# Kernel optimization log

Hardware: AMD Instinct MI355X
Metric: run time of the kernel (lower is better)

Reference implementation:

```python
import jax, jax.numpy as jnp
import numpy as np

H = 50  # hidden_layer_size

def _lstm_layer(x, Wih, Whh, bih, bhh):
    # x: [B, T, D_in]; Wih: [4H, D_in]; Whh: [4H, H]; biases: [4H]
    # Precompute input contribution to all gates for every timestep.
    xg = jnp.einsum('btd,gd->btg', x, Wih) + bih + bhh  # [B, T, 4H]
    xg = jnp.transpose(xg, (1, 0, 2))                   # [T, B, 4H] for scan
    B = x.shape[0]
    h0 = jnp.zeros((B, H), x.dtype)
    c0 = jnp.zeros((B, H), x.dtype)

    def step(carry, xt):
        h, c = carry
        g = xt + h @ Whh.T                              # [B, 4H]
        i, f, gg, o = jnp.split(g, 4, axis=-1)          # PyTorch gate order i,f,g,o
        i = jax.nn.sigmoid(i)
        f = jax.nn.sigmoid(f)
        gg = jnp.tanh(gg)
        o = jax.nn.sigmoid(o)
        c = f * c + i * gg
        h = o * jnp.tanh(c)
        return (h, c), h

    (_, _), hs = jax.lax.scan(step, (h0, c0), xg)       # hs: [T, B, H]
    return jnp.transpose(hs, (1, 0, 2))                 # [B, T, H]


def setup_inputs() -> dict:
    key = jax.random.key(0)
    ks = jax.random.split(key, 11)
    B, T, D = 4096, 512, 1
    s = 1.0 / np.sqrt(H)  # PyTorch LSTM init scale
    inp = {
        'x': jax.random.normal(ks[0], (B, T, D), jnp.float32),
        'W_ih0': jax.random.uniform(ks[1], (4 * H, D), jnp.float32, -s, s),
        'W_hh0': jax.random.uniform(ks[2], (4 * H, H), jnp.float32, -s, s),
        'b_ih0': jax.random.uniform(ks[3], (4 * H,), jnp.float32, -s, s),
        'b_hh0': jax.random.uniform(ks[4], (4 * H,), jnp.float32, -s, s),
        'W_ih1': jax.random.uniform(ks[5], (4 * H, H), jnp.float32, -s, s),
        'W_hh1': jax.random.uniform(ks[6], (4 * H, H), jnp.float32, -s, s),
        'b_ih1': jax.random.uniform(ks[7], (4 * H,), jnp.float32, -s, s),
        'b_hh1': jax.random.uniform(ks[8], (4 * H,), jnp.float32, -s, s),
        'fc_W': jax.random.uniform(ks[9], (1, H), jnp.float32, -s, s),
        'fc_b': jax.random.uniform(ks[10], (1,), jnp.float32, -s, s),
    }
    return inp


def reference(x, W_ih0, W_hh0, b_ih0, b_hh0, W_ih1, W_hh1, b_ih1, b_hh1, fc_W, fc_b):
    h1 = _lstm_layer(x, W_ih0, W_hh0, b_ih0, b_hh0)     # [B, T, H]
    h2 = _lstm_layer(h1, W_ih1, W_hh1, b_ih1, b_hh1)    # [B, T, H]
    last = h2[:, -1, :]                                 # [B, H]
    return last @ fc_W.T + fc_b                         # [B, 1]
```

## Files before the change

kernel.cpp:

```cpp
#include <hip/hip_runtime.h>


typedef __attribute__((ext_vector_type(8))) _Float16 half8;
typedef __attribute__((ext_vector_type(4))) float f32x4;

#define LOG2E 1.44269504088896340736f

__device__ __forceinline__ float rcp_(float x) { return __builtin_amdgcn_rcpf(x); }
__device__ __forceinline__ float exp2_(float x) { return __builtin_amdgcn_exp2f(x); }
__device__ __forceinline__ float sigm(float x) {
  return rcp_(1.f + exp2_(-LOG2E * x));
}
__device__ __forceinline__ float tanh_(float x) {
  return 1.f - 2.f * rcp_(1.f + exp2_(2.f * LOG2E * x));
}
__device__ __forceinline__ f32x4 mfma16(half8 a, half8 b, f32x4 c) {
  return __builtin_amdgcn_mfma_f32_16x16x32_f16(a, b, c, 0, 0, 0);
}

union ABu16 { uint4 u; half8 v; };
__device__ __forceinline__ half8 rdfrag(const _Float16* p) {
  ABu16 t;
  t.u = *(const uint4*)p;
  return t.v;
}

__device__ __forceinline__ half8 loadW1(const float* __restrict__ W, int n,
                                        int gate, int kbase, int lg) {
  half8 r;
#pragma unroll
  for (int e = 0; e < 8; ++e) {
    const int k = kbase + 16 * (e >> 2) + 4 * lg + (e & 3);
    const bool v = (n < 50) && (k < 50);
    r[e] = (_Float16)(v ? W[(gate * 50 + n) * 50 + k] : 0.f);
  }
  return r;
}

#define GATES(X) X(0) X(1) X(2) X(3)

#define FINR(r, PH, WPc)                                      \
  {                                                           \
    const float i_ = sigm(ai[r]), ff = sigm(af[r]);           \
    const float g_ = tanh_(ag[r]), o_ = sigm(ao[r]);          \
    cc##r = ff * cc##r + i_ * g_;                             \
    PH[WPc][woff + 8 * (r)] = (_Float16)(o_ * tanh_(cc##r));  \
  }

__global__ __launch_bounds__(512) void lstm2_kernel(
    const float* __restrict__ x,
    const float* __restrict__ Wih0, const float* __restrict__ Whh0,
    const float* __restrict__ bih0, const float* __restrict__ bhh0,
    const float* __restrict__ Wih1, const float* __restrict__ Whh1,
    const float* __restrict__ bih1, const float* __restrict__ bhh1,
    const float* __restrict__ fcW, const float* __restrict__ fcb,
    float* __restrict__ out) {
  const int tid = threadIdx.x;
  const int lane = tid & 63;
  const int wv = tid >> 6;
  const int wg = wv & 3;
  const bool isL1 = wv >= 4;
  const int lg = lane >> 4;
  const int l15 = lane & 15;
  const int bbase = blockIdx.x * 16;

  __shared__ __align__(16) _Float16 H0[2][1024], H1[2][1024];
  __shared__ float xs2[64][16];
  __shared__ float ldspad[18688];

  ((volatile float*)ldspad)[tid] = 0.f;

  for (int i = tid; i < 1024; i += 512) {
    ((unsigned int*)H0)[i] = 0u;
    ((unsigned int*)H1)[i] = 0u;
  }

  const int lane8 = lane * 8;
  const int u = 16 * wg + l15;
  const bool uv = (u < 50);
  const int woff = ((u >> 5) << 9) + (((u >> 2) & 3) << 7) + ((4 * lg) << 3) +
                   (((u >> 4) & 1) << 2) + (u & 3);

#define STAGE(c)                                                        \
  {                                                                     \
    const int b_ = tid >> 4, fg_ = tid & 15;                            \
    const float4 v_ = *(const float4*)&x[(size_t)(bbase + b_) * 512 +   \
                                         (c) * 64 + 4 * fg_];           \
    xs2[4 * fg_ + 0][b_] = v_.x; xs2[4 * fg_ + 1][b_] = v_.y;           \
    xs2[4 * fg_ + 2][b_] = v_.z; xs2[4 * fg_ + 3][b_] = v_.w;           \
  }

  if (!isL1) {
#define DECL0(G) half8 W0_##G, W1_##G; float bi_##G = 0.f, wx_##G = 0.f;
    GATES(DECL0)
#define LOAD0(G)                                              \
    { W0_##G = loadW1(Whh0, u, G, 0, lg);                     \
      W1_##G = loadW1(Whh0, u, G, 32, lg);                    \
      if (uv) {                                               \
        bi_##G = bih0[G * 50 + u] + bhh0[G * 50 + u];         \
        wx_##G = Wih0[G * 50 + u];                            \
      } }
    GATES(LOAD0)
    float cc0 = 0.f, cc1 = 0.f, cc2 = 0.f, cc3 = 0.f;

#define MM0(G, ACC)                                           \
    ACC = mfma16(f0, W0_##G, ACC);                            \
    ACC = mfma16(f1, W1_##G, ACC);

#define L0STEP(RP, WP, tm)                                                  \
    { const half8 f0 = rdfrag(&H0[RP][lane8]);                              \
      const half8 f1 = rdfrag(&H0[RP][512 + lane8]);                        \
      const float4 xv = *(const float4*)&xs2[tm][4 * lg];                   \
      f32x4 ai = {fmaf(xv.x, wx_0, bi_0), fmaf(xv.y, wx_0, bi_0),           \
                  fmaf(xv.z, wx_0, bi_0), fmaf(xv.w, wx_0, bi_0)};          \
      f32x4 af = {fmaf(xv.x, wx_1, bi_1), fmaf(xv.y, wx_1, bi_1),           \
                  fmaf(xv.z, wx_1, bi_1), fmaf(xv.w, wx_1, bi_1)};          \
      f32x4 ag = {fmaf(xv.x, wx_2, bi_2), fmaf(xv.y, wx_2, bi_2),           \
                  fmaf(xv.z, wx_2, bi_2), fmaf(xv.w, wx_2, bi_2)};          \
      f32x4 ao = {fmaf(xv.x, wx_3, bi_3), fmaf(xv.y, wx_3, bi_3),           \
                  fmaf(xv.z, wx_3, bi_3), fmaf(xv.w, wx_3, bi_3)};          \
      MM0(0, ai) MM0(1, af) MM0(2, ag) MM0(3, ao)                           \
      FINR(0, H0, WP) FINR(1, H0, WP) FINR(2, H0, WP) FINR(3, H0, WP) }

    STAGE(0) __syncthreads();
    L0STEP(1, 0, 0) __syncthreads();
    for (int it = 0; it < 255; ++it) {
      const int todd = 2 * it + 1;
      L0STEP(0, 1, (todd & 63)) __syncthreads();
      const int tev = todd + 1;
      if ((tev & 63) == 0) { STAGE(tev >> 6) __syncthreads(); }
      L0STEP(1, 0, (tev & 63)) __syncthreads();
    }
    L0STEP(0, 1, 63) __syncthreads();
    __syncthreads();
  } else {
#define DECL1(G) half8 I0_##G, I1_##G, R0_##G, R1_##G; float bi_##G = 0.f;
    GATES(DECL1)
#define LOAD1(G)                                              \
    { I0_##G = loadW1(Wih1, u, G, 0, lg);                     \
      I1_##G = loadW1(Wih1, u, G, 32, lg);                    \
      R0_##G = loadW1(Whh1, u, G, 0, lg);                     \
      R1_##G = loadW1(Whh1, u, G, 32, lg);                    \
      if (uv) bi_##G = bih1[G * 50 + u] + bhh1[G * 50 + u]; }
    GATES(LOAD1)
    float cc0 = 0.f, cc1 = 0.f, cc2 = 0.f, cc3 = 0.f;

#define MM1(G, ACC)                                           \
    ACC = mfma16(f0, I0_##G, ACC);                            \
    ACC = mfma16(f1, I1_##G, ACC);                            \
    ACC = mfma16(g0, R0_##G, ACC);                            \
    ACC = mfma16(g1, R1_##G, ACC);

#define L1STEP(P0, R1p, W1p)                                                \
    { const half8 f0 = rdfrag(&H0[P0][lane8]);                              \
      const half8 f1 = rdfrag(&H0[P0][512 + lane8]);                        \
      const half8 g0 = rdfrag(&H1[R1p][lane8]);                             \
      const half8 g1 = rdfrag(&H1[R1p][512 + lane8]);                       \
      f32x4 ai = {bi_0, bi_0, bi_0, bi_0};                                  \
      f32x4 af = {bi_1, bi_1, bi_1, bi_1};                                  \
      f32x4 ag = {bi_2, bi_2, bi_2, bi_2};                                  \
      f32x4 ao = {bi_3, bi_3, bi_3, bi_3};                                  \
      MM1(0, ai) MM1(1, af) MM1(2, ag) MM1(3, ao)                           \
      FINR(0, H1, W1p) FINR(1, H1, W1p) FINR(2, H1, W1p) FINR(3, H1, W1p) }

    __syncthreads(); __syncthreads();
    for (int it = 0; it < 255; ++it) {
      L1STEP(0, 1, 0) __syncthreads();
      if (((2 * it + 2) & 63) == 0) __syncthreads();
      L1STEP(1, 0, 1) __syncthreads();
    }
    L1STEP(0, 1, 0) __syncthreads();
    L1STEP(1, 0, 1) __syncthreads();
  }

  if (tid < 16) {
    float s = fcb[0];
    for (int j = 0; j < 50; ++j) {
      const int idx = ((j >> 5) << 9) + (((j >> 2) & 3) << 7) + (tid << 3) +
                      (((j >> 4) & 1) << 2) + (j & 3);
      s += fcW[j] * (float)H1[1][idx];
    }
    out[bbase + tid] = s;
  }
}

extern "C" void kernel_launch(void* const* d_in, const int* in_sizes, int n_in,
                              void* d_out, int out_size, void* d_ws, size_t ws_size,
                              hipStream_t stream) {
  const float* x    = (const float*)d_in[0];
  const float* Wih0 = (const float*)d_in[1];
  const float* Whh0 = (const float*)d_in[2];
  const float* bih0 = (const float*)d_in[3];
  const float* bhh0 = (const float*)d_in[4];
  const float* Wih1 = (const float*)d_in[5];
  const float* Whh1 = (const float*)d_in[6];
  const float* bih1 = (const float*)d_in[7];
  const float* bhh1 = (const float*)d_in[8];
  const float* fcW  = (const float*)d_in[9];
  const float* fcb  = (const float*)d_in[10];
  float* out = (float*)d_out;

  const int B = out_size;
  const int blocks = B / 16;
  lstm2_kernel<<<dim3(blocks), dim3(512), 0, stream>>>(
      x, Wih0, Whh0, bih0, bhh0, Wih1, Whh1, bih1, bhh1, fcW, fcb, out);
}
```

Baseline: 393.6 us.

## Split layer-1 input projection into separate wave group pipelined through LDS

Adds a third set of four waves per block that computes the layer-1 input projection (Wih1·h0) one timestep ahead and hands it through a double-buffered LDS buffer. The layer-1 recurrent waves then do only the Whh1 matmuls and the gate math, which shortens the per-step critical path that every barrier waits on. Layer 0 now seeds its accumulators with the bias and adds the x·Wih0 term after the MFMAs. The cost is a 768-thread block, one extra pipeline stage, and extra LDS traffic.

After: 390.4 us (median of 2 runs). Within noise of the previous version (-0.8%).

```diff
diff --git a/kernel.cpp b/kernel.cpp
--- a/kernel.cpp
+++ b/kernel.cpp
@@ -37,17 +37,7 @@
   return r;
 }
 
-#define GATES(X) X(0) X(1) X(2) X(3)
-
-#define FINR(r, PH, WPc)                                      \
-  {                                                           \
-    const float i_ = sigm(ai[r]), ff = sigm(af[r]);           \
-    const float g_ = tanh_(ag[r]), o_ = sigm(ao[r]);          \
-    cc##r = ff * cc##r + i_ * g_;                             \
-    PH[WPc][woff + 8 * (r)] = (_Float16)(o_ * tanh_(cc##r));  \
-  }
-
-__global__ __launch_bounds__(512) void lstm2_kernel(
+__global__ __launch_bounds__(768) void lstm2_kernel(
     const float* __restrict__ x,
     const float* __restrict__ Wih0, const float* __restrict__ Whh0,
     const float* __restrict__ bih0, const float* __restrict__ bhh0,
@@ -58,19 +48,20 @@
   const int tid = threadIdx.x;
   const int lane = tid & 63;
   const int wv = tid >> 6;
+  const int role = wv >> 2;
   const int wg = wv & 3;
-  const bool isL1 = wv >= 4;
   const int lg = lane >> 4;
   const int l15 = lane & 15;
   const int bbase = blockIdx.x * 16;
 
   __shared__ __align__(16) _Float16 H0[2][1024], H1[2][1024];
+  __shared__ __align__(16) float Pbuf[2][4096];
   __shared__ float xs2[64][16];
-  __shared__ float ldspad[18688];
+  __shared__ float ldspad[10240];
 
   ((volatile float*)ldspad)[tid] = 0.f;
 
-  for (int i = tid; i < 1024; i += 512) {
+  for (int i = tid; i < 1024; i += 768) {
     ((unsigned int*)H0)[i] = 0u;
     ((unsigned int*)H1)[i] = 0u;
   }
@@ -80,6 +71,7 @@
   const bool uv = (u < 50);
   const int woff = ((u >> 5) << 9) + (((u >> 2) & 3) << 7) + ((4 * lg) << 3) +
                    (((u >> 4) & 1) << 2) + (u & 3);
+  const int pidx = wg * 256 + lane * 4;
 
 #define STAGE(c)                                                        \
   {                                                                     \
@@ -90,87 +82,127 @@
     xs2[4 * fg_ + 2][b_] = v_.z; xs2[4 * fg_ + 3][b_] = v_.w;           \
   }
 
-  if (!isL1) {
-#define DECL0(G) half8 W0_##G, W1_##G; float bi_##G = 0.f, wx_##G = 0.f;
-    GATES(DECL0)
-#define LOAD0(G)                                              \
-    { W0_##G = loadW1(Whh0, u, G, 0, lg);                     \
-      W1_##G = loadW1(Whh0, u, G, 32, lg);                    \
-      if (uv) {                                               \
-        bi_##G = bih0[G * 50 + u] + bhh0[G * 50 + u];         \
-        wx_##G = Wih0[G * 50 + u];                            \
-      } }
-    GATES(LOAD0)
+  if (role == 0) {
+    half8 W0_0, W1_0, W0_1, W1_1, W0_2, W1_2, W0_3, W1_3;
+    float bi_0 = 0.f, bi_1 = 0.f, bi_2 = 0.f, bi_3 = 0.f;
+    float wx_0 = 0.f, wx_1 = 0.f, wx_2 = 0.f, wx_3 = 0.f;
+    W0_0 = loadW1(Whh0, u, 0, 0, lg);  W1_0 = loadW1(Whh0, u, 0, 32, lg);
+    W0_1 = loadW1(Whh0, u, 1, 0, lg);  W1_1 = loadW1(Whh0, u, 1, 32, lg);
+    W0_2 = loadW1(Whh0, u, 2, 0, lg);  W1_2 = loadW1(Whh0, u, 2, 32, lg);
+    W0_3 = loadW1(Whh0, u, 3, 0, lg);  W1_3 = loadW1(Whh0, u, 3, 32, lg);
+    if (uv) {
+      bi_0 = bih0[0 * 50 + u] + bhh0[0 * 50 + u]; wx_0 = Wih0[0 * 50 + u];
+      bi_1 = bih0[1 * 50 + u] + bhh0[1 * 50 + u]; wx_1 = Wih0[1 * 50 + u];
+      bi_2 = bih0[2 * 50 + u] + bhh0[2 * 50 + u]; wx_2 = Wih0[2 * 50 + u];
+      bi_3 = bih0[3 * 50 + u] + bhh0[3 * 50 + u]; wx_3 = Wih0[3 * 50 + u];
+    }
     float cc0 = 0.f, cc1 = 0.f, cc2 = 0.f, cc3 = 0.f;
 
-#define MM0(G, ACC)                                           \
-    ACC = mfma16(f0, W0_##G, ACC);                            \
-    ACC = mfma16(f1, W1_##G, ACC);
-
-#define L0STEP(RP, WP, tm)                                                  \
-    { const half8 f0 = rdfrag(&H0[RP][lane8]);                              \
-      const half8 f1 = rdfrag(&H0[RP][512 + lane8]);                        \
-      const float4 xv = *(const float4*)&xs2[tm][4 * lg];                   \
-      f32x4 ai = {fmaf(xv.x, wx_0, bi_0), fmaf(xv.y, wx_0, bi_0),           \
-                  fmaf(xv.z, wx_0, bi_0), fmaf(xv.w, wx_0, bi_0)};          \
-      f32x4 af = {fmaf(xv.x, wx_1, bi_1), fmaf(xv.y, wx_1, bi_1),           \
-                  fmaf(xv.z, wx_1, bi_1), fmaf(xv.w, wx_1, bi_1)};          \
-      f32x4 ag = {fmaf(xv.x, wx_2, bi_2), fmaf(xv.y, wx_2, bi_2),           \
-                  fmaf(xv.z, wx_2, bi_2), fmaf(xv.w, wx_2, bi_2)};          \
-      f32x4 ao = {fmaf(xv.x, wx_3, bi_3), fmaf(xv.y, wx_3, bi_3),           \
-                  fmaf(xv.z, wx_3, bi_3), fmaf(xv.w, wx_3, bi_3)};          \
-      MM0(0, ai) MM0(1, af) MM0(2, ag) MM0(3, ao)                           \
-      FINR(0, H0, WP) FINR(1, H0, WP) FINR(2, H0, WP) FINR(3, H0, WP) }
-
-    STAGE(0) __syncthreads();
-    L0STEP(1, 0, 0) __syncthreads();
-    for (int it = 0; it < 255; ++it) {
-      const int todd = 2 * it + 1;
-      L0STEP(0, 1, (todd & 63)) __syncthreads();
-      const int tev = todd + 1;
-      if ((tev & 63) == 0) { STAGE(tev >> 6) __syncthreads(); }
-      L0STEP(1, 0, (tev & 63)) __syncthreads();
-    }
-    L0STEP(0, 1, 63) __syncthreads();
-    __syncthreads();
+#define FIN0(r, xr, WPc)                                              \
+    { const float i_ = sigm(ai[r] + (xr) * wx_0);                     \
+      const float ff = sigm(af[r] + (xr) * wx_1);                     \
+      const float g_ = tanh_(ag[r] + (xr) * wx_2);                    \
+      const float o_ = sigm(ao[r] + (xr) * wx_3);                     \
+      cc##r = ff * cc##r + i_ * g_;                                   \
+      H0[WPc][woff + 8 * (r)] = (_Float16)(o_ * tanh_(cc##r)); }
+
+#define L0STEP(RP, WP, tm)                                            \
+    { const half8 f0 = rdfrag(&H0[RP][lane8]);                        \
+      const half8 f1 = rdfrag(&H0[RP][512 + lane8]);                  \
+      f32x4 ai = {bi_0, bi_0, bi_0, bi_0};                            \
+      f32x4 af = {bi_1, bi_1, bi_1, bi_1};                            \
+      f32x4 ag = {bi_2, bi_2, bi_2, bi_2};                            \
+      f32x4 ao = {bi_3, bi_3, bi_3, bi_3};                            \
+      ai = mfma16(f0, W0_0, ai); ai = mfma16(f1, W1_0, ai);           \
+      af = mfma16(f0, W0_1, af); af = mfma16(f1, W1_1, af);           \
+      ag = mfma16(f0, W0_2, ag); ag = mfma16(f1, W1_2, ag);           \
+      ao = mfma16(f0, W0_3, ao); ao = mfma16(f1, W1_3, ao);           \
+      const float4 xv = *(const float4*)&xs2[tm][4 * lg];             \
+      FIN0(0, xv.x, WP) FIN0(1, xv.y, WP)                             \
+      FIN0(2, xv.z, WP) FIN0(3, xv.w, WP) }
+
+    for (int it = 0; it <= 256; ++it) {
+      if ((it & 31) == 0 && it < 256) { STAGE(it >> 5) __syncthreads(); }
+      if (it < 256) L0STEP(1, 0, ((2 * it) & 63))
+      __syncthreads();
+      if (it < 256) L0STEP(0, 1, ((2 * it + 1) & 63))
+      __syncthreads();
+    }
+  } else if (role == 1) {
+    half8 I0_0, I1_0, I0_1, I1_1, I0_2, I1_2, I0_3, I1_3;
+    I0_0 = loadW1(Wih1, u, 0, 0, lg);  I1_0 = loadW1(Wih1, u, 0, 32, lg);
+    I0_1 = loadW1(Wih1, u, 1, 0, lg);  I1_1 = loadW1(Wih1, u, 1, 32, lg);
+    I0_2 = loadW1(Wih1, u, 2, 0, lg);  I1_2 = loadW1(Wih1, u, 2, 32, lg);
+    I0_3 = loadW1(Wih1, u, 3, 0, lg);  I1_3 = loadW1(Wih1, u, 3, 32, lg);
+
+#define ISTEP(RP, WPp)                                                \
+    { const half8 f0 = rdfrag(&H0[RP][lane8]);                        \
+      const half8 f1 = rdfrag(&H0[RP][512 + lane8]);                  \
+      f32x4 a0 = {0.f, 0.f, 0.f, 0.f};                                \
+      f32x4 a1 = a0, a2 = a0, a3 = a0;                                \
+      a0 = mfma16(f0, I0_0, a0); a0 = mfma16(f1, I1_0, a0);           \
+      a1 = mfma16(f0, I0_1, a1); a1 = mfma16(f1, I1_1, a1);           \
+      a2 = mfma16(f0, I0_2, a2); a2 = mfma16(f1, I1_2, a2);           \
+      a3 = mfma16(f0, I0_3, a3); a3 = mfma16(f1, I1_3, a3);           \
+      *(f32x4*)&Pbuf[WPp][pidx]        = a0;                          \
+      *(f32x4*)&Pbuf[WPp][1024 + pidx] = a1;                          \
+      *(f32x4*)&Pbuf[WPp][2048 + pidx] = a2;                          \
+      *(f32x4*)&Pbuf[WPp][3072 + pidx] = a3; }
+
+    for (int it = 0; it <= 256; ++it) {
+      if ((it & 31) == 0 && it < 256) { __syncthreads(); }
+      if (it >= 1) ISTEP(1, 1)
+      __syncthreads();
+      if (it < 256) ISTEP(0, 0)
+      __syncthreads();
+    }
   } else {
-#define DECL1(G) half8 I0_##G, I1_##G, R0_##G, R1_##G; float bi_##G = 0.f;
-    GATES(DECL1)
-#define LOAD1(G)                                              \
-    { I0_##G = loadW1(Wih1, u, G, 0, lg);                     \
-      I1_##G = loadW1(Wih1, u, G, 32, lg);                    \
-      R0_##G = loadW1(Whh1, u, G, 0, lg);                     \
-      R1_##G = loadW1(Whh1, u, G, 32, lg);                    \
-      if (uv) bi_##G = bih1[G * 50 + u] + bhh1[G * 50 + u]; }
-    GATES(LOAD1)
+    half8 R0_0, R1_0, R0_1, R1_1, R0_2, R1_2, R0_3, R1_3;
+    float bi_0 = 0.f, bi_1 = 0.f, bi_2 = 0.f, bi_3 = 0.f;
+    R0_0 = loadW1(Whh1, u, 0, 0, lg);  R1_0 = loadW1(Whh1, u, 0, 32, lg);
+    R0_1 = loadW1(Whh1, u, 1, 0, lg);  R1_1 = loadW1(Whh1, u, 1, 32, lg);
+    R0_2 = loadW1(Whh1, u, 2, 0, lg);  R1_2 = loadW1(Whh1, u, 2, 32, lg);
+    R0_3 = loadW1(Whh1, u, 3, 0, lg);  R1_3 = loadW1(Whh1, u, 3, 32, lg);
+    if (uv) {
+      bi_0 = bih1[0 * 50 + u] + bhh1[0 * 50 + u];
+      bi_1 = bih1[1 * 50 + u] + bhh1[1 * 50 + u];
+      bi_2 = bih1[2 * 50 + u] + bhh1[2 * 50 + u];
+      bi_3 = bih1[3 * 50 + u] + bhh1[3 * 50 + u];
+    }
     float cc0 = 0.f, cc1 = 0.f, cc2 = 0.f, cc3 = 0.f;
 
-#define MM1(G, ACC)                                           \
-    ACC = mfma16(f0, I0_##G, ACC);                            \
-    ACC = mfma16(f1, I1_##G, ACC);                            \
-    ACC = mfma16(g0, R0_##G, ACC);                            \
-    ACC = mfma16(g1, R1_##G, ACC);
-
-#define L1STEP(P0, R1p, W1p)                                                \
-    { const half8 f0 = rdfrag(&H0[P0][lane8]);                              \
-      const half8 f1 = rdfrag(&H0[P0][512 + lane8]);                        \
-      const half8 g0 = rdfrag(&H1[R1p][lane8]);                             \
-      const half8 g1 = rdfrag(&H1[R1p][512 + lane8]);                       \
-      f32x4 ai = {bi_0, bi_0, bi_0, bi_0};                                  \
-      f32x4 af = {bi_1, bi_1, bi_1, bi_1};                                  \
-      f32x4 ag = {bi_2, bi_2, bi_2, bi_2};                                  \
-      f32x4 ao = {bi_3, bi_3, bi_3, bi_3};                                  \
-      MM1(0, ai) MM1(1, af) MM1(2, ag) MM1(3, ao)                           \
-      FINR(0, H1, W1p) FINR(1, H1, W1p) FINR(2, H1, W1p) FINR(3, H1, W1p) }
-
-    __syncthreads(); __syncthreads();
-    for (int it = 0; it < 255; ++it) {
-      L1STEP(0, 1, 0) __syncthreads();
-      if (((2 * it + 2) & 63) == 0) __syncthreads();
-      L1STEP(1, 0, 1) __syncthreads();
-    }
-    L1STEP(0, 1, 0) __syncthreads();
-    L1STEP(1, 0, 1) __syncthreads();
+#define FINR2(r, WH)                                                  \
+    { const float i_ = sigm(ai[r] + p0[r]);                           \
+      const float ff = sigm(af[r] + p1[r]);                           \
+      const float g_ = tanh_(ag[r] + p2[r]);                          \
+      const float o_ = sigm(ao[r] + p3[r]);                           \
+      cc##r = ff * cc##r + i_ * g_;                                   \
+      H1[WH][woff + 8 * (r)] = (_Float16)(o_ * tanh_(cc##r)); }
+
+#define RSTEP(PP, RH, WH)                                             \
+    { const half8 g0 = rdfrag(&H1[RH][lane8]);                        \
+      const half8 g1 = rdfrag(&H1[RH][512 + lane8]);                  \
+      const f32x4 p0 = *(const f32x4*)&Pbuf[PP][pidx];                \
+      const f32x4 p1 = *(const f32x4*)&Pbuf[PP][1024 + pidx];         \
+      const f32x4 p2 = *(const f32x4*)&Pbuf[PP][2048 + pidx];         \
+      const f32x4 p3 = *(const f32x4*)&Pbuf[PP][3072 + pidx];         \
+      f32x4 ai = {bi_0, bi_0, bi_0, bi_0};                            \
+      f32x4 af = {bi_1, bi_1, bi_1, bi_1};                            \
+      f32x4 ag = {bi_2, bi_2, bi_2, bi_2};                            \
+      f32x4 ao = {bi_3, bi_3, bi_3, bi_3};                            \
+      ai = mfma16(g0, R0_0, ai); ai = mfma16(g1, R1_0, ai);           \
+      af = mfma16(g0, R0_1, af); af = mfma16(g1, R1_1, af);           \
+      ag = mfma16(g0, R0_2, ag); ag = mfma16(g1, R1_2, ag);           \
+      ao = mfma16(g0, R0_3, ao); ao = mfma16(g1, R1_3, ao);           \
+      FINR2(0, WH) FINR2(1, WH) FINR2(2, WH) FINR2(3, WH) }
+
+    for (int it = 0; it <= 256; ++it) {
+      if ((it & 31) == 0 && it < 256) { __syncthreads(); }
+      if (it >= 1) RSTEP(0, 1, 0)
+      __syncthreads();
+      if (it >= 1) RSTEP(1, 0, 1)
+      __syncthreads();
+    }
   }
 
   if (tid < 16) {
@@ -202,6 +234,6 @@
 
   const int B = out_size;
   const int blocks = B / 16;
-  lstm2_kernel<<<dim3(blocks), dim3(512), 0, stream>>>(
+  lstm2_kernel<<<dim3(blocks), dim3(768), 0, stream>>>(
       x, Wih0, Whh0, bih0, bhh0, Wih1, Whh1, bih1, bhh1, fcW, fcb, out);
 }
```
